# Performance work log

Measured on AMD Instinct MI355X. Metric: run time of the kernel, lower is better.

Reference implementation:

```python
import jax, jax.numpy as jnp
import numpy as np

N, H, W = 128, 128, 128
K = 9          # 3x3 kernel points
DIL = 3        # dilation of the deformable conv


def conv2d(x, w, pad, dil):
    # x: [N,C,H,W], w: [O,I,kh,kw]
    return jax.lax.conv_general_dilated(
        x, w, (1, 1), [(pad, pad), (pad, pad)], rhs_dilation=(dil, dil),
        dimension_numbers=("NCHW", "OIHW", "NCHW"))


def _bilinear_one(img, py, px):
    # img: [C,H,W]; py, px: [K,H,W] sample coords. Zero outside borders (DCNv2 semantics).
    Hh, Ww = img.shape[1], img.shape[2]
    y0f = jnp.floor(py)
    x0f = jnp.floor(px)
    y0 = y0f.astype(jnp.int32)
    x0 = x0f.astype(jnp.int32)
    ly = (py - y0f)[None]   # [1,K,H,W]
    lx = (px - x0f)[None]

    def gather(yi, xi):
        valid = ((yi >= 0) & (yi < Hh) & (xi >= 0) & (xi < Ww)).astype(img.dtype)
        yc = jnp.clip(yi, 0, Hh - 1)
        xc = jnp.clip(xi, 0, Ww - 1)
        return img[:, yc, xc] * valid[None]   # [C,K,H,W]

    v00 = gather(y0, x0)
    v01 = gather(y0, x0 + 1)
    v10 = gather(y0 + 1, x0)
    v11 = gather(y0 + 1, x0 + 1)
    return (v00 * (1 - ly) * (1 - lx) + v01 * (1 - ly) * lx
            + v10 * ly * (1 - lx) + v11 * ly * lx)


def modulated_deform_conv(x, offset, mod, w, b):
    # x: [N,C,H,W]; offset: [N,2K,H,W] with (dy,dx) interleaved per kernel point
    # (standard DCNv2 channel layout); mod: [N,K,H,W]; w: [O,C,3,3]; b: [O]
    Np, C, Hh, Ww = x.shape
    dy = offset[:, 0::2]   # [N,K,H,W]
    dx = offset[:, 1::2]
    base_y = ((jnp.repeat(jnp.arange(3), 3) - 1) * DIL).astype(x.dtype)  # [K]
    base_x = ((jnp.tile(jnp.arange(3), 3) - 1) * DIL).astype(x.dtype)
    gy = jnp.arange(Hh, dtype=x.dtype).reshape(1, 1, Hh, 1)
    gx = jnp.arange(Ww, dtype=x.dtype).reshape(1, 1, 1, Ww)
    py = dy + base_y.reshape(1, K, 1, 1) + gy   # [N,K,H,W]
    px = dx + base_x.reshape(1, K, 1, 1) + gx
    samp = jax.vmap(_bilinear_one)(x, py, px)   # [N,C,K,H,W]
    samp = samp * mod[:, None]                  # sigmoid modulation
    out = jnp.einsum("nckij,ock->noij", samp, w.reshape(w.shape[0], C, K))
    return out + b.reshape(1, -1, 1, 1)


def setup_inputs() -> dict:
    key = jax.random.key(0)
    ks = jax.random.split(key, 12)
    f32 = jnp.float32
    return {
        "mask": jax.random.normal(ks[0], (N, 1, H, W), f32),
        "x": jax.random.normal(ks[1], (N, 8, H, W), f32),
        "w1": jax.random.normal(ks[2], (2, 9, 3, 3), f32) * 0.1,      # conv1x1_1 (3x3)
        "b1": jnp.zeros((2,), f32),
        "w_off": jax.random.normal(ks[3], (27, 2, 3, 3), f32) * 0.05,  # offset/mask conv
        "w_dcn": jax.random.normal(ks[4], (2, 2, 3, 3), f32) * 0.2,    # deform conv weight
        "b_dcn": jnp.zeros((2,), f32),
        "w2": jax.random.normal(ks[5], (2, 2, 1, 1), f32) * 0.5,       # conv1x1_2
        "b2": jnp.zeros((2,), f32),
        "fc1_w": jax.random.normal(ks[6], (2048, 2 * 64 * 64), f32) * 0.01,
        "fc1_b": jnp.zeros((2048,), f32),
        "fc2_w": jax.random.normal(ks[7], (1024, 2048), f32) * 0.02,
        "fc2_b": jnp.zeros((1024,), f32),
        "io_w": jax.random.normal(ks[8], (1, 1024), f32) * 0.01,
        "io_b": jnp.zeros((1,), f32),
    }


def reference(mask, x, w1, b1, w_off, w_dcn, b_dcn, w2, b2,
              fc1_w, fc1_b, fc2_w, fc2_b, io_w, io_b):
    z = jnp.concatenate([x, mask], axis=1)                    # [N,9,H,W]
    h = conv2d(z, w1, 1, 1) + b1.reshape(1, -1, 1, 1)          # [N,2,H,W]
    om = conv2d(h, w_off, 3, 3)                               # [N,27,H,W], bias=False
    ox, oy, mm = jnp.split(om, 3, axis=1)
    offset = jnp.concatenate([ox, oy], axis=1)                # [N,18,H,W]
    mm = jax.nn.sigmoid(mm)                                   # [N,9,H,W]
    h = modulated_deform_conv(h, offset, mm, w_dcn, b_dcn)    # [N,2,H,W]
    h = jax.nn.relu(conv2d(h, w2, 0, 1) + b2.reshape(1, -1, 1, 1))
    Np, C, Hh, Ww = h.shape                                   # adaptive max pool to 64x64
    h = h.reshape(Np, C, 64, Hh // 64, 64, Ww // 64).max(axis=(3, 5))
    h = h.reshape(Np, -1)                                     # [N, 8192]
    h = jax.nn.relu(h @ fc1_w.T + fc1_b)
    h = jax.nn.relu(h @ fc2_w.T + fc2_b)
    return jax.nn.sigmoid(h @ io_w.T + io_b)                  # [N,1]
```

## Files before the change

### kernel.cpp

```cpp
#include <hip/hip_runtime.h>
#include <math.h>

#define NB   128
#define HH   128
#define WW   128
#define HW   (HH*WW)
#define POOLD 64
#define FC1_IN  8192
#define FC1_OUT 2048
#define FC2_OUT 1024

#define H1_OFF    0
#define POOL_OFF  4194304
#define FC1_OFF   5242880
#define FC2_OFF   5505024

__global__ __launch_bounds__(256) void conv1_kernel(
    const float* __restrict__ xin, const float* __restrict__ mask,
    const float* __restrict__ w1, const float* __restrict__ b1,
    float* __restrict__ h1)
{
    __shared__ float sw[164];
    __shared__ float sh[9][10][132];

    int tid = threadIdx.x;
    int n   = blockIdx.y;
    int r0  = blockIdx.x * 8;

    if (tid < 162) sw[tid] = w1[tid];
    if (tid < 2)   sw[162 + tid] = b1[tid];

    for (int i = tid; i < 90; i += 256) {
        int c  = i / 10;
        int ry = i - c * 10;
        sh[c][ry][0]   = 0.f;
        sh[c][ry][129] = 0.f;
    }

    for (int idx = tid; idx < 2880; idx += 256) {
        int c   = idx / 320;
        int rem = idx - c * 320;
        int ry  = rem >> 5;
        int x4  = (rem & 31) << 2;
        int g   = r0 - 1 + ry;
        float4 v = make_float4(0.f, 0.f, 0.f, 0.f);
        if (g >= 0 && g < HH) {
            const float* src = (c < 8) ? (xin + ((size_t)n * 8 + c) * HW)
                                       : (mask + (size_t)n * HW);
            v = *(const float4*)(src + (size_t)g * WW + x4);
        }
        float* d = &sh[c][ry][x4 + 1];
        d[0] = v.x; d[1] = v.y; d[2] = v.z; d[3] = v.w;
    }
    __syncthreads();

    int x  = tid & 127;
    int yb = (tid >> 7) * 4;

    float acc[4][2];
    #pragma unroll
    for (int r = 0; r < 4; ++r) { acc[r][0] = sw[162]; acc[r][1] = sw[163]; }

    for (int c = 0; c < 9; ++c) {
        float v[6][3];
        #pragma unroll
        for (int iy = 0; iy < 6; ++iy)
            #pragma unroll
            for (int kx = 0; kx < 3; ++kx)
                v[iy][kx] = sh[c][yb + iy][x + kx];
        #pragma unroll
        for (int r = 0; r < 4; ++r)
            #pragma unroll
            for (int ky = 0; ky < 3; ++ky)
                #pragma unroll
                for (int kx = 0; kx < 3; ++kx) {
                    float t = v[r + ky][kx];
                    acc[r][0] += t * sw[c * 9 + ky * 3 + kx];
                    acc[r][1] += t * sw[81 + c * 9 + ky * 3 + kx];
                }
    }

    #pragma unroll
    for (int r = 0; r < 4; ++r) {
        size_t base = (size_t)n * (2 * HW) + (size_t)(r0 + yb + r) * WW + x;
        h1[base]      = acc[r][0];
        h1[base + HW] = acc[r][1];
    }
}

#define HALO 8

__device__ __forceinline__ void fetch2(
    const float* __restrict__ sh, const float* __restrict__ h0,
    const float* __restrict__ hb, int row_lo, int row_hi,
    int yi, int xi, float& a, float& b)
{
    a = 0.f; b = 0.f;
    if (yi < 0 || yi >= HH || xi < 0 || xi >= WW) return;
    if (yi >= row_lo && yi < row_hi) {
        const float* p = sh + ((size_t)(yi - row_lo) * WW + xi) * 2;
        a = p[0]; b = p[1];
    } else {
        a = h0[yi * WW + xi];
        b = hb[yi * WW + xi];
    }
}

__global__ __launch_bounds__(256, 4) void fused_dcn_kernel(
    const float* __restrict__ h1,
    const float* __restrict__ w_off,
    const float* __restrict__ w_dcn,
    const float* __restrict__ b_dcn,
    const float* __restrict__ w2,
    const float* __restrict__ b2,
    float* __restrict__ pooled)
{
    __shared__ float sh[32 * WW * 2];
    __shared__ float sw[530];

    int tid = threadIdx.x;
    int n   = blockIdx.y;
    int r0  = blockIdx.x * 16;

    for (int i = tid; i < 530; i += 256) {
        float v;
        if (i < 486)      v = w_off[i];
        else if (i < 522) v = w_dcn[i - 486];
        else if (i < 526) v = w2[i - 522];
        else if (i < 528) v = b_dcn[i - 526];
        else              v = b2[i - 528];
        sw[i] = v;
    }

    int row_lo = r0 - HALO;       if (row_lo < 0)   row_lo = 0;
    int row_hi = r0 + 16 + HALO;  if (row_hi > HH)  row_hi = HH;
    int rows = row_hi - row_lo;

    const float* h0 = h1 + (size_t)n * (2 * HW);
    const float* hb = h0 + HW;

    for (int idx = tid; idx < rows * 32; idx += 256) {
        int ry = idx >> 5;
        int x4 = (idx & 31) << 2;
        const float4 a = *(const float4*)(h0 + (size_t)(row_lo + ry) * WW + x4);
        const float4 b = *(const float4*)(hb + (size_t)(row_lo + ry) * WW + x4);
        float* d = sh + ((size_t)ry * WW + x4) * 2;
        d[0] = a.x; d[1] = b.x; d[2] = a.y; d[3] = b.y;
        d[4] = a.z; d[5] = b.z; d[6] = a.w; d[7] = b.w;
    }
    __syncthreads();

    const float* WOFF = sw;
    const float* WDCN = sw + 486;
    const float* W2   = sw + 522;
    const float* BDCN = sw + 526;
    const float* B2   = sw + 528;

    int pc  = tid & 63;
    int prb = blockIdx.x * 8 + (tid >> 6);

    #pragma unroll 1
    for (int i = 0; i < 2; ++i) {
        int pr = prb + 4 * i;
        float m0 = -1e30f, m1 = -1e30f;

        #pragma unroll 1
        for (int s = 0; s < 4; ++s) {
            int y = pr * 2 + (s >> 1);
            int x = pc * 2 + (s & 1);

            float hvx[9], hvy[9];
            #pragma unroll
            for (int t = 0; t < 9; ++t) {
                int yy = y + (t / 3 - 1) * 3;
                int xx = x + (t % 3 - 1) * 3;
                float a = 0.f, b = 0.f;
                if (yy >= 0 && yy < HH && xx >= 0 && xx < WW) {
                    const float* p = sh + ((size_t)(yy - row_lo) * WW + xx) * 2;
                    a = p[0]; b = p[1];
                }
                hvx[t] = a; hvy[t] = b;
            }

            float acc0 = 0.f, acc1 = 0.f;
            #pragma unroll 1
            for (int k = 0; k < 9; ++k) {
                const float* wy = WOFF + (2 * k) * 18;
                const float* wx = WOFF + (2 * k + 1) * 18;
                const float* wm = WOFF + (18 + k) * 18;
                float dyv = 0.f, dxv = 0.f, mv = 0.f;
                #pragma unroll
                for (int t = 0; t < 9; ++t) {
                    float ha = hvx[t], hcb = hvy[t];
                    dyv += ha * wy[t] + hcb * wy[9 + t];
                    dxv += ha * wx[t] + hcb * wx[9 + t];
                    mv  += ha * wm[t] + hcb * wm[9 + t];
                }
                float mod = 1.f / (1.f + __expf(-mv));

                float py  = (float)(y + (k / 3 - 1) * 3) + dyv;
                float pxx = (float)(x + (k % 3 - 1) * 3) + dxv;
                float y0f = floorf(py), x0f = floorf(pxx);
                int   y0 = (int)y0f,   x0 = (int)x0f;
                float ly = py - y0f,   lx = pxx - x0f;

                float a00, b00, a01, b01, a10, b10, a11, b11;
                fetch2(sh, h0, hb, row_lo, row_hi, y0,     x0,     a00, b00);
                fetch2(sh, h0, hb, row_lo, row_hi, y0,     x0 + 1, a01, b01);
                fetch2(sh, h0, hb, row_lo, row_hi, y0 + 1, x0,     a10, b10);
                fetch2(sh, h0, hb, row_lo, row_hi, y0 + 1, x0 + 1, a11, b11);

                float w00 = (1.f - ly) * (1.f - lx);
                float w01 = (1.f - ly) * lx;
                float w10 = ly * (1.f - lx);
                float w11 = ly * lx;
                float sA = (w00 * a00 + w01 * a01 + w10 * a10 + w11 * a11) * mod;
                float sB = (w00 * b00 + w01 * b01 + w10 * b10 + w11 * b11) * mod;

                acc0 += WDCN[k]      * sA + WDCN[9 + k]  * sB;
                acc1 += WDCN[18 + k] * sA + WDCN[27 + k] * sB;
            }

            float v0 = acc0 + BDCN[0];
            float v1 = acc1 + BDCN[1];
            float u0 = fmaxf(W2[0] * v0 + W2[1] * v1 + B2[0], 0.f);
            float u1 = fmaxf(W2[2] * v0 + W2[3] * v1 + B2[1], 0.f);
            m0 = fmaxf(m0, u0);
            m1 = fmaxf(m1, u1);
        }

        size_t pb = (size_t)n * FC1_IN + (size_t)pr * POOLD + pc;
        pooled[pb]        = m0;
        pooled[pb + 4096] = m1;
    }
}

__global__ void init_bias2_kernel(
    float* __restrict__ o1, const float* __restrict__ bb1,
    float* __restrict__ o2, const float* __restrict__ bb2)
{
    int i = blockIdx.x * blockDim.x + threadIdx.x;
    if (i < NB * FC1_OUT) o1[i] = bb1[i & (FC1_OUT - 1)];
    if (i < NB * FC2_OUT) o2[i] = bb2[i & (FC2_OUT - 1)];
}

typedef __bf16 bf16x8 __attribute__((ext_vector_type(8)));
typedef float  f32x4  __attribute__((ext_vector_type(4)));

#define LDT 40

__device__ __forceinline__ unsigned short f2bf(float f) {
    unsigned int u = __float_as_uint(f);
    return (unsigned short)((u + 0x7fffu + ((u >> 16) & 1u)) >> 16);
}

__global__ __launch_bounds__(256) void gemm_bf16_splitk(
    const float* __restrict__ A, const float* __restrict__ B,
    float* __restrict__ C, int K, int Nc, int kchunk, int relu_a)
{
    __shared__ __align__(16) unsigned short As[128 * LDT];
    __shared__ __align__(16) unsigned short Bs[64 * LDT];

    int tid = threadIdx.x;
    int jt  = blockIdx.x;
    int k0  = blockIdx.y * kchunk;
    int iters = kchunk >> 5;

    int t8  = tid >> 3;
    int c16 = (tid & 7) << 2;

    const float* Ag = A + (size_t)t8 * K + k0 + c16;
    const float* Bg = B + (size_t)(jt * 64 + t8) * K + k0 + c16;

    float4 pa[4]; float4 pb[2];
    #pragma unroll
    for (int p = 0; p < 4; ++p) pa[p] = *(const float4*)(Ag + (size_t)(p * 32) * K);
    #pragma unroll
    for (int p = 0; p < 2; ++p) pb[p] = *(const float4*)(Bg + (size_t)(p * 32) * K);

    int lane = tid & 63;
    int w    = tid >> 6;
    int quad = lane >> 4;
    int r    = lane & 15;

    f32x4 acc[2][4];
    #pragma unroll
    for (int mt = 0; mt < 2; ++mt)
        #pragma unroll
        for (int nt = 0; nt < 4; ++nt)
            acc[mt][nt] = (f32x4){0.f, 0.f, 0.f, 0.f};

    for (int it = 0; it < iters; ++it) {
        #pragma unroll
        for (int p = 0; p < 4; ++p) {
            float4 v = pa[p];
            if (relu_a) {
                v.x = fmaxf(v.x, 0.f); v.y = fmaxf(v.y, 0.f);
                v.z = fmaxf(v.z, 0.f); v.w = fmaxf(v.w, 0.f);
            }
            ushort4 s = make_ushort4(f2bf(v.x), f2bf(v.y), f2bf(v.z), f2bf(v.w));
            *(ushort4*)&As[(t8 + p * 32) * LDT + c16] = s;
        }
        #pragma unroll
        for (int p = 0; p < 2; ++p) {
            float4 v = pb[p];
            ushort4 s = make_ushort4(f2bf(v.x), f2bf(v.y), f2bf(v.z), f2bf(v.w));
            *(ushort4*)&Bs[(t8 + p * 32) * LDT + c16] = s;
        }
        __syncthreads();

        if (it + 1 < iters) {
            Ag += 32; Bg += 32;
            #pragma unroll
            for (int p = 0; p < 4; ++p) pa[p] = *(const float4*)(Ag + (size_t)(p * 32) * K);
            #pragma unroll
            for (int p = 0; p < 2; ++p) pb[p] = *(const float4*)(Bg + (size_t)(p * 32) * K);
        }

        bf16x8 af[2];
        #pragma unroll
        for (int mt = 0; mt < 2; ++mt)
            af[mt] = *(const bf16x8*)&As[(w * 32 + mt * 16 + r) * LDT + quad * 8];
        bf16x8 bfr[4];
        #pragma unroll
        for (int nt = 0; nt < 4; ++nt)
            bfr[nt] = *(const bf16x8*)&Bs[(nt * 16 + r) * LDT + quad * 8];

        #pragma unroll
        for (int mt = 0; mt < 2; ++mt)
            #pragma unroll
            for (int nt = 0; nt < 4; ++nt)
                acc[mt][nt] = __builtin_amdgcn_mfma_f32_16x16x32_bf16(
                    af[mt], bfr[nt], acc[mt][nt], 0, 0, 0);

        __syncthreads();
    }

    #pragma unroll
    for (int mt = 0; mt < 2; ++mt) {
        int mrow = w * 32 + mt * 16 + quad * 4;
        #pragma unroll
        for (int nt = 0; nt < 4; ++nt) {
            int col = jt * 64 + nt * 16 + r;
            #pragma unroll
            for (int i = 0; i < 4; ++i)
                atomicAdd(C + (size_t)(mrow + i) * Nc + col, acc[mt][nt][i]);
        }
    }
}

__global__ __launch_bounds__(256) void io_kernel(
    const float* __restrict__ fc2o, const float* __restrict__ io_w,
    const float* __restrict__ io_b, float* __restrict__ out)
{
    int n = blockIdx.x;
    int tid = threadIdx.x;
    float s = 0.f;
    #pragma unroll
    for (int k = tid; k < FC2_OUT; k += 256)
        s += fmaxf(fc2o[(size_t)n * FC2_OUT + k], 0.f) * io_w[k];
    #pragma unroll
    for (int off = 32; off > 0; off >>= 1)
        s += __shfl_down(s, off, 64);
    __shared__ float red[4];
    if ((tid & 63) == 0) red[tid >> 6] = s;
    __syncthreads();
    if (tid == 0) {
        float t = red[0] + red[1] + red[2] + red[3] + io_b[0];
        out[n] = 1.f / (1.f + expf(-t));
    }
}

extern "C" void kernel_launch(void* const* d_in, const int* in_sizes, int n_in,
                              void* d_out, int out_size, void* d_ws, size_t ws_size,
                              hipStream_t stream)
{
    const float* mask  = (const float*)d_in[0];
    const float* x     = (const float*)d_in[1];
    const float* w1    = (const float*)d_in[2];
    const float* b1    = (const float*)d_in[3];
    const float* w_off = (const float*)d_in[4];
    const float* w_dcn = (const float*)d_in[5];
    const float* b_dcn = (const float*)d_in[6];
    const float* w2    = (const float*)d_in[7];
    const float* b2    = (const float*)d_in[8];
    const float* fc1_w = (const float*)d_in[9];
    const float* fc1_b = (const float*)d_in[10];
    const float* fc2_w = (const float*)d_in[11];
    const float* fc2_b = (const float*)d_in[12];
    const float* io_w  = (const float*)d_in[13];
    const float* io_b  = (const float*)d_in[14];

    float* ws      = (float*)d_ws;
    float* h1      = ws + H1_OFF;
    float* pooled  = ws + POOL_OFF;
    float* fc1_out = ws + FC1_OFF;
    float* fc2_out = ws + FC2_OFF;
    float* out     = (float*)d_out;

    conv1_kernel<<<dim3(16, NB), 256, 0, stream>>>(x, mask, w1, b1, h1);

    fused_dcn_kernel<<<dim3(8, NB), 256, 0, stream>>>(
        h1, w_off, w_dcn, b_dcn, w2, b2, pooled);

    init_bias2_kernel<<<(NB * FC1_OUT + 255) / 256, 256, 0, stream>>>(
        fc1_out, fc1_b, fc2_out, fc2_b);

    gemm_bf16_splitk<<<dim3(FC1_OUT / 64, 16), 256, 0, stream>>>(
        pooled, fc1_w, fc1_out, FC1_IN, FC1_OUT, FC1_IN / 16, 0);

    gemm_bf16_splitk<<<dim3(FC2_OUT / 64, 16), 256, 0, stream>>>(
        fc1_out, fc2_w, fc2_out, FC1_OUT, FC2_OUT, FC1_OUT / 16, 1);

    io_kernel<<<NB, 256, 0, stream>>>(fc2_out, io_w, io_b, out);
}
```

Measured before the change: 330.8 us.

## Shrink DCN tile to zero-padded halo buffer with fast-path bilinear fetch

The fused DCN kernel now processes 8 output rows per block instead of 16, doubling the grid, and stages an 18x140 zero-padded tile in shared memory. The smaller footprint (about 20KB instead of 32KB) lets the occupancy hint rise from 4 to 7 blocks. With the zero padding, the 3x3 neighbourhood reads need no bounds checks. Bilinear samples with small offsets read the four corners straight from shared memory, and larger offsets fall back to guarded global loads. The costs are more redundant halo loads per output row and a branch on offset size that may diverge within a wavefront.

```diff
diff --git a/kernel.cpp b/kernel.cpp
--- a/kernel.cpp
+++ b/kernel.cpp
@@ -88,25 +88,23 @@
     }
 }
 
-#define HALO 8
-
-__device__ __forceinline__ void fetch2(
-    const float* __restrict__ sh, const float* __restrict__ h0,
-    const float* __restrict__ hb, int row_lo, int row_hi,
+#define HALO_Y 5
+#define HALO_X 6
+#define SROWS  18
+#define SCOLS  140
+
+__device__ __forceinline__ void fetchg(
+    const float* __restrict__ h0, const float* __restrict__ hb,
     int yi, int xi, float& a, float& b)
 {
     a = 0.f; b = 0.f;
-    if (yi < 0 || yi >= HH || xi < 0 || xi >= WW) return;
-    if (yi >= row_lo && yi < row_hi) {
-        const float* p = sh + ((size_t)(yi - row_lo) * WW + xi) * 2;
-        a = p[0]; b = p[1];
-    } else {
+    if ((unsigned)yi < (unsigned)HH && (unsigned)xi < (unsigned)WW) {
         a = h0[yi * WW + xi];
         b = hb[yi * WW + xi];
     }
 }
 
-__global__ __launch_bounds__(256, 4) void fused_dcn_kernel(
+__global__ __launch_bounds__(256, 7) void fused_dcn_kernel(
     const float* __restrict__ h1,
     const float* __restrict__ w_off,
     const float* __restrict__ w_dcn,
@@ -115,12 +113,12 @@
     const float* __restrict__ b2,
     float* __restrict__ pooled)
 {
-    __shared__ float sh[32 * WW * 2];
+    __shared__ __align__(16) float sh[SROWS * SCOLS * 2];
     __shared__ float sw[530];
 
     int tid = threadIdx.x;
     int n   = blockIdx.y;
-    int r0  = blockIdx.x * 16;
+    int r0  = blockIdx.x * 8;
 
     for (int i = tid; i < 530; i += 256) {
         float v;
@@ -132,21 +130,24 @@
         sw[i] = v;
     }
 
-    int row_lo = r0 - HALO;       if (row_lo < 0)   row_lo = 0;
-    int row_hi = r0 + 16 + HALO;  if (row_hi > HH)  row_hi = HH;
-    int rows = row_hi - row_lo;
+    for (int i = tid; i < (SROWS * SCOLS * 2) / 4; i += 256)
+        ((float4*)sh)[i] = make_float4(0.f, 0.f, 0.f, 0.f);
+    __syncthreads();
 
     const float* h0 = h1 + (size_t)n * (2 * HW);
     const float* hb = h0 + HW;
 
-    for (int idx = tid; idx < rows * 32; idx += 256) {
+    for (int idx = tid; idx < SROWS * 32; idx += 256) {
         int ry = idx >> 5;
         int x4 = (idx & 31) << 2;
-        const float4 a = *(const float4*)(h0 + (size_t)(row_lo + ry) * WW + x4);
-        const float4 b = *(const float4*)(hb + (size_t)(row_lo + ry) * WW + x4);
-        float* d = sh + ((size_t)ry * WW + x4) * 2;
-        d[0] = a.x; d[1] = b.x; d[2] = a.y; d[3] = b.y;
-        d[4] = a.z; d[5] = b.z; d[6] = a.w; d[7] = b.w;
+        int g  = r0 - HALO_Y + ry;
+        if (g >= 0 && g < HH) {
+            const float4 a = *(const float4*)(h0 + (size_t)g * WW + x4);
+            const float4 b = *(const float4*)(hb + (size_t)g * WW + x4);
+            float* d = sh + ((size_t)ry * SCOLS + HALO_X + x4) * 2;
+            ((float4*)d)[0] = make_float4(a.x, b.x, a.y, b.y);
+            ((float4*)d)[1] = make_float4(a.z, b.z, a.w, b.w);
+        }
     }
     __syncthreads();
 
@@ -156,83 +157,83 @@
     const float* BDCN = sw + 526;
     const float* B2   = sw + 528;
 
-    int pc  = tid & 63;
-    int prb = blockIdx.x * 8 + (tid >> 6);
+    int pc = tid & 63;
+    int pr = blockIdx.x * 4 + (tid >> 6);
+
+    float m0 = -1e30f, m1 = -1e30f;
 
     #pragma unroll 1
-    for (int i = 0; i < 2; ++i) {
-        int pr = prb + 4 * i;
-        float m0 = -1e30f, m1 = -1e30f;
-
+    for (int s = 0; s < 4; ++s) {
+        int y = pr * 2 + (s >> 1);
+        int x = pc * 2 + (s & 1);
+
+        const float* tb = sh + ((size_t)(y - r0 + HALO_Y) * SCOLS + (x + HALO_X)) * 2;
+        float hvx[9], hvy[9];
+        #pragma unroll
+        for (int t = 0; t < 9; ++t) {
+            const float* p = tb + ((t / 3 - 1) * 3 * SCOLS + (t % 3 - 1) * 3) * 2;
+            hvx[t] = p[0]; hvy[t] = p[1];
+        }
+
+        float acc0 = 0.f, acc1 = 0.f;
         #pragma unroll 1
-        for (int s = 0; s < 4; ++s) {
-            int y = pr * 2 + (s >> 1);
-            int x = pc * 2 + (s & 1);
-
-            float hvx[9], hvy[9];
+        for (int k = 0; k < 9; ++k) {
+            const float* wy = WOFF + (2 * k) * 18;
+            const float* wx = WOFF + (2 * k + 1) * 18;
+            const float* wm = WOFF + (18 + k) * 18;
+            float dyv = 0.f, dxv = 0.f, mv = 0.f;
             #pragma unroll
             for (int t = 0; t < 9; ++t) {
-                int yy = y + (t / 3 - 1) * 3;
-                int xx = x + (t % 3 - 1) * 3;
-                float a = 0.f, b = 0.f;
-                if (yy >= 0 && yy < HH && xx >= 0 && xx < WW) {
-                    const float* p = sh + ((size_t)(yy - row_lo) * WW + xx) * 2;
-                    a = p[0]; b = p[1];
-                }
-                hvx[t] = a; hvy[t] = b;
+                float ha = hvx[t], hcb = hvy[t];
+                dyv += ha * wy[t] + hcb * wy[9 + t];
+                dxv += ha * wx[t] + hcb * wx[9 + t];
+                mv  += ha * wm[t] + hcb * wm[9 + t];
             }
-
-            float acc0 = 0.f, acc1 = 0.f;
-            #pragma unroll 1
-            for (int k = 0; k < 9; ++k) {
-                const float* wy = WOFF + (2 * k) * 18;
-                const float* wx = WOFF + (2 * k + 1) * 18;
-                const float* wm = WOFF + (18 + k) * 18;
-                float dyv = 0.f, dxv = 0.f, mv = 0.f;
-                #pragma unroll
-                for (int t = 0; t < 9; ++t) {
-                    float ha = hvx[t], hcb = hvy[t];
-                    dyv += ha * wy[t] + hcb * wy[9 + t];
-                    dxv += ha * wx[t] + hcb * wx[9 + t];
-                    mv  += ha * wm[t] + hcb * wm[9 + t];
-                }
-                float mod = 1.f / (1.f + __expf(-mv));
-
-                float py  = (float)(y + (k / 3 - 1) * 3) + dyv;
-                float pxx = (float)(x + (k % 3 - 1) * 3) + dxv;
-                float y0f = floorf(py), x0f = floorf(pxx);
-                int   y0 = (int)y0f,   x0 = (int)x0f;
-                float ly = py - y0f,   lx = pxx - x0f;
-
-                float a00, b00, a01, b01, a10, b10, a11, b11;
-                fetch2(sh, h0, hb, row_lo, row_hi, y0,     x0,     a00, b00);
-                fetch2(sh, h0, hb, row_lo, row_hi, y0,     x0 + 1, a01, b01);
-                fetch2(sh, h0, hb, row_lo, row_hi, y0 + 1, x0,     a10, b10);
-                fetch2(sh, h0, hb, row_lo, row_hi, y0 + 1, x0 + 1, a11, b11);
-
-                float w00 = (1.f - ly) * (1.f - lx);
-                float w01 = (1.f - ly) * lx;
-                float w10 = ly * (1.f - lx);
-                float w11 = ly * lx;
-                float sA = (w00 * a00 + w01 * a01 + w10 * a10 + w11 * a11) * mod;
-                float sB = (w00 * b00 + w01 * b01 + w10 * b10 + w11 * b11) * mod;
-
-                acc0 += WDCN[k]      * sA + WDCN[9 + k]  * sB;
-                acc1 += WDCN[18 + k] * sA + WDCN[27 + k] * sB;
+            float mod = 1.f / (1.f + __expf(-mv));
+
+            float py  = (float)(y + (k / 3 - 1) * 3) + dyv;
+            float pxx = (float)(x + (k % 3 - 1) * 3) + dxv;
+            float y0f = floorf(py), x0f = floorf(pxx);
+            int   y0 = (int)y0f,   x0 = (int)x0f;
+            float ly = py - y0f,   lx = pxx - x0f;
+
+            float a00, b00, a01, b01, a10, b10, a11, b11;
+            if (fabsf(dyv) < 2.0f && fabsf(dxv) < 3.0f) {
+                const float* p = sh + ((size_t)(y0 - r0 + HALO_Y) * SCOLS
+                                       + (x0 + HALO_X)) * 2;
+                a00 = p[0];             b00 = p[1];
+                a01 = p[2];             b01 = p[3];
+                a10 = p[SCOLS * 2];     b10 = p[SCOLS * 2 + 1];
+                a11 = p[SCOLS * 2 + 2]; b11 = p[SCOLS * 2 + 3];
+            } else {
+                fetchg(h0, hb, y0,     x0,     a00, b00);
+                fetchg(h0, hb, y0,     x0 + 1, a01, b01);
+                fetchg(h0, hb, y0 + 1, x0,     a10, b10);
+                fetchg(h0, hb, y0 + 1, x0 + 1, a11, b11);
             }
 
-            float v0 = acc0 + BDCN[0];
-            float v1 = acc1 + BDCN[1];
-            float u0 = fmaxf(W2[0] * v0 + W2[1] * v1 + B2[0], 0.f);
-            float u1 = fmaxf(W2[2] * v0 + W2[3] * v1 + B2[1], 0.f);
-            m0 = fmaxf(m0, u0);
-            m1 = fmaxf(m1, u1);
-        }
-
-        size_t pb = (size_t)n * FC1_IN + (size_t)pr * POOLD + pc;
-        pooled[pb]        = m0;
-        pooled[pb + 4096] = m1;
-    }
+            float w00 = (1.f - ly) * (1.f - lx);
+            float w01 = (1.f - ly) * lx;
+            float w10 = ly * (1.f - lx);
+            float w11 = ly * lx;
+            float sA = (w00 * a00 + w01 * a01 + w10 * a10 + w11 * a11) * mod;
+            float sB = (w00 * b00 + w01 * b01 + w10 * b10 + w11 * b11) * mod;
+
+            acc0 += WDCN[k]      * sA + WDCN[9 + k]  * sB;
+            acc1 += WDCN[18 + k] * sA + WDCN[27 + k] * sB;
+        }
+
+        float v0 = acc0 + BDCN[0];
+        float v1 = acc1 + BDCN[1];
+        float u0 = fmaxf(W2[0] * v0 + W2[1] * v1 + B2[0], 0.f);
+        float u1 = fmaxf(W2[2] * v0 + W2[3] * v1 + B2[1], 0.f);
+        m0 = fmaxf(m0, u0);
+        m1 = fmaxf(m1, u1);
+    }
+
+    size_t pb = (size_t)n * FC1_IN + (size_t)pr * POOLD + pc;
+    pooled[pb]        = m0;
+    pooled[pb + 4096] = m1;
 }
 
 __global__ void init_bias2_kernel(
@@ -400,7 +401,7 @@
 
     conv1_kernel<<<dim3(16, NB), 256, 0, stream>>>(x, mask, w1, b1, h1);
 
-    fused_dcn_kernel<<<dim3(8, NB), 256, 0, stream>>>(
+    fused_dcn_kernel<<<dim3(16, NB), 256, 0, stream>>>(
         h1, w_off, w_dcn, b_dcn, w2, b2, pooled);
 
     init_bias2_kernel<<<(NB * FC1_OUT + 255) / 256, 256, 0, stream>>>(
```

New measurement: 377.4 us. 14.1% more time.
